# Kernel tuning notes

Measured on AMD Instinct MI355X. Metric: run time of the kernel, lower is better.

The kernel has to match this reference:

```python
import jax, jax.numpy as jnp
import numpy as np
from jax import lax

TEMPERATURE = 30.0
BN_EPS = 1e-5


def setup_inputs() -> dict:
    key = jax.random.key(0)
    ks = jax.random.split(key, 9)
    B, H, W, C_in = 32, 64, 64, 128
    n_filters, r_filters, n_kernels = 128, 4, 4
    x = jax.random.normal(ks[0], (B, H, W, C_in), dtype=jnp.float32)
    reduction_kernel = jax.random.normal(ks[1], (C_in, r_filters), dtype=jnp.float32) * 0.02
    attention_kernel = jax.random.normal(ks[2], (r_filters, n_kernels), dtype=jnp.float32) * 0.02
    conv_kernels = jax.random.normal(ks[3], (n_kernels, 3, 3, C_in, n_filters), dtype=jnp.float32) * 0.05
    bias = jax.random.normal(ks[4], (n_kernels, n_filters), dtype=jnp.float32) * 0.05
    bn_scale = jax.random.uniform(ks[5], (n_filters,), dtype=jnp.float32, minval=0.5, maxval=1.5)
    bn_bias = jax.random.normal(ks[6], (n_filters,), dtype=jnp.float32) * 0.1
    bn_mean = jax.random.normal(ks[7], (n_filters,), dtype=jnp.float32) * 0.1
    bn_var = jax.random.uniform(ks[8], (n_filters,), dtype=jnp.float32, minval=0.5, maxval=1.5)
    return {"x": x, "reduction_kernel": reduction_kernel, "attention_kernel": attention_kernel,
            "conv_kernels": conv_kernels, "bias": bias, "bn_scale": bn_scale, "bn_bias": bn_bias,
            "bn_mean": bn_mean, "bn_var": bn_var}


def reference(x, reduction_kernel, attention_kernel, conv_kernels, bias, bn_scale, bn_bias, bn_mean, bn_var):
    # x: [B,H,W,C_in] NHWC. Inference mode (training=False): BN uses running stats.
    B = x.shape[0]
    # Squeeze-style routing: global average pool -> reduce -> relu -> attention over experts.
    pool = jnp.mean(x, axis=(1, 2))                             # [B, C_in]
    pool_red = jax.nn.relu(pool @ reduction_kernel)             # [B, r]
    attention = jax.nn.softmax((pool_red @ attention_kernel) / TEMPERATURE, axis=-1)  # [B, K]
    # Soft mixture of conv expert kernels, per sample.
    w_mixed = jnp.einsum('bk,khwio->bhwio', attention, conv_kernels)  # [B,kH,kW,C_in,F]

    def per_sample_conv(xi, wi):
        # xi: [H,W,C_in], wi: [kH,kW,C_in,F]
        return lax.conv_general_dilated(xi[None], wi, window_strides=(1, 1), padding='SAME',
                                        dimension_numbers=('NHWC', 'HWIO', 'NHWC'))[0]

    y = jax.vmap(per_sample_conv)(x, w_mixed)                   # [B,H,W,F]
    b_mixed = attention @ bias                                  # [B, F]
    y = y + b_mixed[:, None, None, :]
    # BatchNorm (inference) + relu
    inv = bn_scale * lax.rsqrt(bn_var + BN_EPS)
    y = (y - bn_mean) * inv + bn_bias
    return jax.nn.relu(y)
```

## Files before the change

### kernel.cpp

```cpp
#include <hip/hip_runtime.h>

typedef short bf16x8 __attribute__((ext_vector_type(8)));
typedef float f32x4 __attribute__((ext_vector_type(4)));
typedef unsigned int u32x4 __attribute__((ext_vector_type(4)));
typedef unsigned short u16x4 __attribute__((ext_vector_type(4)));

__device__ __forceinline__ unsigned short f2bf(float f) {
  unsigned u = __builtin_bit_cast(unsigned, f);
  u = (u + 0x7FFFu + ((u >> 16) & 1u)) >> 16;
  return (unsigned short)u;
}

__global__ __launch_bounds__(256) void k_pool_cvt(const float* __restrict__ x,
                                                  unsigned short* __restrict__ xb,
                                                  float* __restrict__ pp) {
  const int slice = blockIdx.x;
  const int b = blockIdx.y;
  const int t = threadIdx.x;
  const int c4 = (t & 31) * 4;
  const int seg = t >> 5;
  const size_t base = ((size_t)b * 4096 + slice * 256 + seg * 32) * 128;
  const float* xp = x + base;
  unsigned short* xbp = xb + base;
  f32x4 s = {0.f, 0.f, 0.f, 0.f};
  for (int p = 0; p < 32; ++p) {
    f32x4 v = *(const f32x4*)(xp + p * 128 + c4);
    s += v;
    u16x4 h;
    h.x = f2bf(v.x); h.y = f2bf(v.y); h.z = f2bf(v.z); h.w = f2bf(v.w);
    *(u16x4*)(xbp + p * 128 + c4) = h;
  }
  __shared__ f32x4 red[256];
  red[t] = s;
  __syncthreads();
  if (t < 32) {
    f32x4 tot = red[t];
#pragma unroll
    for (int g = 1; g < 8; ++g) tot += red[g * 32 + t];
    *(f32x4*)(pp + (size_t)(b * 16 + slice) * 128 + t * 4) = tot;
  }
}

__global__ __launch_bounds__(128) void k_route(const float* __restrict__ pp,
    const float* __restrict__ redk, const float* __restrict__ attk,
    const float* __restrict__ bias, const float* __restrict__ bns,
    const float* __restrict__ bnb, const float* __restrict__ bnm,
    const float* __restrict__ bnv,
    float* __restrict__ att_ws, float* __restrict__ beta_ws,
    float* __restrict__ alpha_ws) {
  const int b = blockIdx.x, t = threadIdx.x;
  __shared__ float pool[128];
  __shared__ float att[4];
  {
    float s = 0.f;
    for (int i = 0; i < 16; ++i) s += pp[(size_t)(b * 16 + i) * 128 + t];
    pool[t] = s * (1.f / 4096.f);
  }
  __syncthreads();
  if (t == 0) {
    float pr[4];
    for (int r = 0; r < 4; ++r) {
      float s = 0.f;
      for (int c = 0; c < 128; ++c) s += pool[c] * redk[c * 4 + r];
      pr[r] = fmaxf(s, 0.f);
    }
    float lgt[4]; float mx = -1e30f;
    for (int k = 0; k < 4; ++k) {
      float s = 0.f;
      for (int r = 0; r < 4; ++r) s += pr[r] * attk[r * 4 + k];
      lgt[k] = s * (1.f / 30.f);
      mx = fmaxf(mx, lgt[k]);
    }
    float den = 0.f;
    for (int k = 0; k < 4; ++k) { lgt[k] = expf(lgt[k] - mx); den += lgt[k]; }
    for (int k = 0; k < 4; ++k) { att[k] = lgt[k] / den; att_ws[b * 4 + k] = att[k]; }
  }
  __syncthreads();
  {
    float bm = 0.f;
    for (int k = 0; k < 4; ++k) bm += att[k] * bias[k * 128 + t];
    const float inv = bns[t] * rsqrtf(bnv[t] + 1e-5f);
    beta_ws[b * 128 + t] = (bm - bnm[t]) * inv + bnb[t];
    alpha_ws[t] = inv;
  }
}

__global__ __launch_bounds__(256) void k_mixw(const float* __restrict__ ck,
                                              const float* __restrict__ att_ws,
                                              unsigned short* __restrict__ w_ws) {
  const int tap = blockIdx.x;
  const int b = blockIdx.y;
  const int t = threadIdx.x;
  const float a0 = att_ws[b * 4 + 0], a1 = att_ws[b * 4 + 1];
  const float a2 = att_ws[b * 4 + 2], a3 = att_ws[b * 4 + 3];
  const float* ckp = ck + (size_t)tap * 16384;
  __shared__ unsigned short lds_t[128 * 136];
#pragma unroll 4
  for (int it = 0; it < 16; ++it) {
    const int i4 = t + it * 256;
    const int idx = i4 * 4;
    const int c = idx >> 7, f = idx & 127;
    f32x4 v0 = *(const f32x4*)(ckp + idx);
    f32x4 v1 = *(const f32x4*)(ckp + idx + 147456);
    f32x4 v2 = *(const f32x4*)(ckp + idx + 2 * 147456);
    f32x4 v3 = *(const f32x4*)(ckp + idx + 3 * 147456);
#pragma unroll
    for (int e = 0; e < 4; ++e)
      lds_t[(f + e) * 136 + c] = f2bf(a0 * v0[e] + a1 * v1[e] + a2 * v2[e] + a3 * v3[e]);
  }
  __syncthreads();
#pragma unroll
  for (int it = 0; it < 8; ++it) {
    const int m = t + it * 256;
    const int f = m >> 4, oo = m & 15, h = oo >> 3, o = oo & 7;
    unsigned short* dst = w_ws + ((size_t)b * 18 + h * 9 + tap) * 8192
                        + (size_t)(f * 8 + (o ^ (f & 7))) * 8;
    *(bf16x8*)dst = *(const bf16x8*)(lds_t + f * 136 + oo * 8);
  }
}

__device__ __forceinline__ void stage_w16(char* dst, const unsigned short* src, int t) {
#pragma unroll
  for (int j = 0; j < 2; ++j) {
    const int i = t + j * 512;
    __builtin_amdgcn_global_load_lds(
        (const __attribute__((address_space(1))) void*)(src + (size_t)i * 8),
        (__attribute__((address_space(3))) void*)(dst + i * 16), 16, 0, 0);
  }
}

__device__ __forceinline__ void stage_x_half(char* xt, const unsigned short* xbp,
                                             int r0, int h, int t) {
  const int pix = t >> 3;
  const int oct = (t & 7) ^ ((t >> 3) & 7);
#pragma unroll
  for (int j = 0; j < 6; ++j) {
    const int rr = r0 - 1 + j;
    char* dst = xt + j * 8192 + t * 16;
    if ((unsigned)rr < 64u) {
      __builtin_amdgcn_global_load_lds(
          (const __attribute__((address_space(1))) void*)
              (xbp + ((size_t)(rr * 64 + pix)) * 128 + h * 64 + oct * 8),
          (__attribute__((address_space(3))) void*)dst, 16, 0, 0);
    } else {
      *(u32x4*)dst = (u32x4){0, 0, 0, 0};
    }
  }
}

__global__ __launch_bounds__(512, 4) void k_conv(const unsigned short* __restrict__ xb,
                                                 const unsigned short* __restrict__ w_ws,
                                                 const float* __restrict__ alpha_ws,
                                                 const float* __restrict__ beta_ws,
                                                 float* __restrict__ out) {
  extern __shared__ char lds[];
  char* xt = lds;
  char* wlds = lds + 49152;

  const int orig = blockIdx.x;
  const int wg = (orig & 7) * 64 + (orig >> 3);
  const int b = wg >> 4;
  const int tile = wg & 15;
  const int t = threadIdx.x;
  const int lane = t & 63, wid = t >> 6;
  const int wm = wid >> 1, wn = wid & 1;
  const int lr = lane & 15, lg = lane >> 4;
  const int r0 = tile * 4;

  const unsigned short* xbp = xb + (size_t)b * 4096 * 128;
  const unsigned short* wsrc = w_ws + (size_t)b * 18 * 8192;

  f32x4 acc[4][4] = {};
  const bf16x8 zero = {};

  stage_x_half(xt, xbp, r0, 0, t);
  stage_w16(wlds, wsrc, t);
  __syncthreads();

  for (int s = 0; s < 18; ++s) {
    const int tap = s % 9;
    char* cb = wlds + ((s & 1) << 14);
    if (s < 17) stage_w16(wlds + (((s & 1) ^ 1) << 14), wsrc + (size_t)(s + 1) * 8192, t);
    const int dh = tap / 3 - 1, dw = tap % 3 - 1;
    const int jrow = wm + dh + 1;
#pragma unroll
    for (int kc = 0; kc < 2; ++kc) {
      bf16x8 afr[4], bfr[4];
#pragma unroll
      for (int mf = 0; mf < 4; ++mf) {
        const int col = mf * 16 + lr + dw;
        const int a = ((jrow * 64 + col) * 128 + kc * 64 + lg * 16) ^ ((col & 7) << 4);
        afr[mf] = ((unsigned)col < 64u) ? *(const bf16x8*)(xt + a) : zero;
      }
#pragma unroll
      for (int nf = 0; nf < 4; ++nf) {
        const int f = wn * 64 + nf * 16 + lr;
        const int a = (f * 128 + kc * 64 + lg * 16) ^ ((f & 7) << 4);
        bfr[nf] = *(const bf16x8*)(cb + a);
      }
#pragma unroll
      for (int mf = 0; mf < 4; ++mf)
#pragma unroll
        for (int nf = 0; nf < 4; ++nf)
          acc[mf][nf] = __builtin_amdgcn_mfma_f32_16x16x32_bf16(afr[mf], bfr[nf],
                                                                acc[mf][nf], 0, 0, 0);
    }
    __syncthreads();
    if (s == 8) {
      stage_x_half(xt, xbp, r0, 1, t);
      __syncthreads();
    }
  }

  float af[4], bt[4];
#pragma unroll
  for (int nf = 0; nf < 4; ++nf) {
    const int f = wn * 64 + nf * 16 + lr;
    af[nf] = alpha_ws[f];
    bt[nf] = beta_ws[b * 128 + f];
  }
  float* op = out + (size_t)b * 4096 * 128;
  const int row = r0 + wm;
#pragma unroll
  for (int mf = 0; mf < 4; ++mf) {
#pragma unroll
    for (int r = 0; r < 4; ++r) {
      const int col = mf * 16 + lg * 4 + r;
#pragma unroll
      for (int nf = 0; nf < 4; ++nf) {
        const int f = wn * 64 + nf * 16 + lr;
        const float v = acc[mf][nf][r] * af[nf] + bt[nf];
        op[(size_t)(row * 64 + col) * 128 + f] = fmaxf(v, 0.f);
      }
    }
  }
}

extern "C" void kernel_launch(void* const* d_in, const int* in_sizes, int n_in,
                              void* d_out, int out_size, void* d_ws, size_t ws_size,
                              hipStream_t stream) {
  const float* x    = (const float*)d_in[0];
  const float* redk = (const float*)d_in[1];
  const float* attk = (const float*)d_in[2];
  const float* ck   = (const float*)d_in[3];
  const float* bias = (const float*)d_in[4];
  const float* bns  = (const float*)d_in[5];
  const float* bnbb = (const float*)d_in[6];
  const float* bnm  = (const float*)d_in[7];
  const float* bnv  = (const float*)d_in[8];
  float* out = (float*)d_out;

  char* ws = (char*)d_ws;
  unsigned short* xb   = (unsigned short*)ws;
  unsigned short* w_ws = (unsigned short*)(ws + 33554432);
  float* pp       = (float*)(ws + 42991616);
  float* att_ws   = (float*)(ws + 43253760);
  float* beta_ws  = (float*)(ws + 43254272);
  float* alpha_ws = (float*)(ws + 43270656);

  k_pool_cvt<<<dim3(16, 32), 256, 0, stream>>>(x, xb, pp);
  k_route<<<32, 128, 0, stream>>>(pp, redk, attk, bias, bns, bnbb, bnm, bnv,
                                  att_ws, beta_ws, alpha_ws);
  k_mixw<<<dim3(9, 32), 256, 0, stream>>>(ck, att_ws, w_ws);
  k_conv<<<512, 512, 81920, stream>>>(xb, w_ws, alpha_ws, beta_ws, out);
}
```

Before: 83.15 us.

## Load conv weights directly from global into registers with double-buffered prefetch

The conv kernel no longer stages mixed weights through LDS. Each wave reads its B fragments straight from global (L2) memory into registers, with a two-deep register prefetch, and the weight workspace is relaid into per-k-chunk 32-element rows to suit this. The tile shrinks to 2 output rows with 256 threads and 1024 blocks, which cuts LDS to 32KB and the per-tap barriers to those around the x-half restage. The cost is more global/L2 traffic for weights, since each block re-reads its sample's full weight set, and exposed global latency if the prefetch does not hide it.

```diff
diff --git a/kernel.cpp b/kernel.cpp
--- a/kernel.cpp
+++ b/kernel.cpp
@@ -109,38 +109,35 @@
       lds_t[(f + e) * 136 + c] = f2bf(a0 * v0[e] + a1 * v1[e] + a2 * v2[e] + a3 * v3[e]);
   }
   __syncthreads();
+  unsigned short* wb = w_ws + (size_t)b * 147456;
 #pragma unroll
   for (int it = 0; it < 8; ++it) {
     const int m = t + it * 256;
-    const int f = m >> 4, oo = m & 15, h = oo >> 3, o = oo & 7;
-    unsigned short* dst = w_ws + ((size_t)b * 18 + h * 9 + tap) * 8192
-                        + (size_t)(f * 8 + (o ^ (f & 7))) * 8;
-    *(bf16x8*)dst = *(const bf16x8*)(lds_t + f * 136 + oo * 8);
-  }
-}
-
-__device__ __forceinline__ void stage_w16(char* dst, const unsigned short* src, int t) {
-#pragma unroll
-  for (int j = 0; j < 2; ++j) {
-    const int i = t + j * 512;
-    __builtin_amdgcn_global_load_lds(
-        (const __attribute__((address_space(1))) void*)(src + (size_t)i * 8),
-        (__attribute__((address_space(3))) void*)(dst + i * 16), 16, 0, 0);
-  }
-}
-
-__device__ __forceinline__ void stage_x_half(char* xt, const unsigned short* xbp,
-                                             int r0, int h, int t) {
-  const int pix = t >> 3;
-  const int oct = (t & 7) ^ ((t >> 3) & 7);
-#pragma unroll
-  for (int j = 0; j < 6; ++j) {
-    const int rr = r0 - 1 + j;
-    char* dst = xt + j * 8192 + t * 16;
+    const int f = m >> 4, o = m & 15;
+    const int h = o >> 3;
+    const int cp = (o & 7) * 8;
+    const int kc = cp >> 5;
+    const int c2 = cp & 31;
+    unsigned short* dst = wb + ((size_t)(((h * 9 + tap) * 2 + kc) * 128 + f)) * 32 + c2;
+    *(bf16x8*)dst = *(const bf16x8*)(lds_t + f * 136 + o * 8);
+  }
+}
+
+__device__ __forceinline__ void stage_x(char* xt, const unsigned short* xbp,
+                                        int r0, int h, int t) {
+#pragma unroll
+  for (int j = 0; j < 8; ++j) {
+    const int i = t + j * 256;
+    const int jr = i >> 9;
+    const int pix = (i & 511) >> 3;
+    const int oct = i & 7;
+    const int soct = oct ^ (pix & 7);
+    const int rr = r0 - 1 + jr;
+    char* dst = xt + i * 16;
     if ((unsigned)rr < 64u) {
       __builtin_amdgcn_global_load_lds(
           (const __attribute__((address_space(1))) void*)
-              (xbp + ((size_t)(rr * 64 + pix)) * 128 + h * 64 + oct * 8),
+              (xbp + ((size_t)(rr * 64 + pix)) * 128 + h * 64 + soct * 8),
           (__attribute__((address_space(3))) void*)dst, 16, 0, 0);
     } else {
       *(u32x4*)dst = (u32x4){0, 0, 0, 0};
@@ -148,66 +145,73 @@
   }
 }
 
-__global__ __launch_bounds__(512, 4) void k_conv(const unsigned short* __restrict__ xb,
+#define LOADB(dst, u)                                                          \
+  {                                                                            \
+    const unsigned short* wp = wsrc + (size_t)(u) * 4096;                      \
+    _Pragma("unroll")                                                          \
+    for (int nf = 0; nf < 4; ++nf) {                                           \
+      const int f = wn * 64 + nf * 16 + lr;                                    \
+      dst[nf] = *(const bf16x8*)(wp + f * 32 + lg * 8);                        \
+    }                                                                          \
+  }
+
+#define COMPUTE(kc, bfr)                                                       \
+  {                                                                            \
+    bf16x8 afr[4];                                                             \
+    _Pragma("unroll")                                                          \
+    for (int mf = 0; mf < 4; ++mf) {                                           \
+      const int col = mf * 16 + lr + dw;                                       \
+      const int a = (((jrow * 64 + col) * 128 + (kc) * 64 + lg * 16))          \
+                    ^ ((col & 7) << 4);                                        \
+      afr[mf] = ((unsigned)col < 64u) ? *(const bf16x8*)(xt + a) : zero;       \
+    }                                                                          \
+    _Pragma("unroll")                                                          \
+    for (int mf = 0; mf < 4; ++mf)                                             \
+      _Pragma("unroll")                                                        \
+      for (int nf = 0; nf < 4; ++nf)                                           \
+        acc[mf][nf] = __builtin_amdgcn_mfma_f32_16x16x32_bf16(afr[mf],         \
+                          bfr[nf], acc[mf][nf], 0, 0, 0);                      \
+  }
+
+__global__ __launch_bounds__(256, 3) void k_conv(const unsigned short* __restrict__ xb,
                                                  const unsigned short* __restrict__ w_ws,
                                                  const float* __restrict__ alpha_ws,
                                                  const float* __restrict__ beta_ws,
                                                  float* __restrict__ out) {
-  extern __shared__ char lds[];
-  char* xt = lds;
-  char* wlds = lds + 49152;
+  __shared__ char xt[32768];
 
   const int orig = blockIdx.x;
-  const int wg = (orig & 7) * 64 + (orig >> 3);
-  const int b = wg >> 4;
-  const int tile = wg & 15;
+  const int wg = (orig & 7) * 128 + (orig >> 3);
+  const int b = wg >> 5;
+  const int tile = wg & 31;
   const int t = threadIdx.x;
   const int lane = t & 63, wid = t >> 6;
   const int wm = wid >> 1, wn = wid & 1;
   const int lr = lane & 15, lg = lane >> 4;
-  const int r0 = tile * 4;
+  const int r0 = tile * 2;
 
   const unsigned short* xbp = xb + (size_t)b * 4096 * 128;
-  const unsigned short* wsrc = w_ws + (size_t)b * 18 * 8192;
+  const unsigned short* wsrc = w_ws + (size_t)b * 147456;
 
   f32x4 acc[4][4] = {};
   const bf16x8 zero = {};
-
-  stage_x_half(xt, xbp, r0, 0, t);
-  stage_w16(wlds, wsrc, t);
-  __syncthreads();
-
-  for (int s = 0; s < 18; ++s) {
-    const int tap = s % 9;
-    char* cb = wlds + ((s & 1) << 14);
-    if (s < 17) stage_w16(wlds + (((s & 1) ^ 1) << 14), wsrc + (size_t)(s + 1) * 8192, t);
+  bf16x8 bA[4], bB[4];
+
+  stage_x(xt, xbp, r0, 0, t);
+  LOADB(bA, 0);
+  __syncthreads();
+
+  for (int u = 0; u < 36; u += 2) {
+    const int tap = (u >> 1) % 9;
     const int dh = tap / 3 - 1, dw = tap % 3 - 1;
     const int jrow = wm + dh + 1;
-#pragma unroll
-    for (int kc = 0; kc < 2; ++kc) {
-      bf16x8 afr[4], bfr[4];
-#pragma unroll
-      for (int mf = 0; mf < 4; ++mf) {
-        const int col = mf * 16 + lr + dw;
-        const int a = ((jrow * 64 + col) * 128 + kc * 64 + lg * 16) ^ ((col & 7) << 4);
-        afr[mf] = ((unsigned)col < 64u) ? *(const bf16x8*)(xt + a) : zero;
-      }
-#pragma unroll
-      for (int nf = 0; nf < 4; ++nf) {
-        const int f = wn * 64 + nf * 16 + lr;
-        const int a = (f * 128 + kc * 64 + lg * 16) ^ ((f & 7) << 4);
-        bfr[nf] = *(const bf16x8*)(cb + a);
-      }
-#pragma unroll
-      for (int mf = 0; mf < 4; ++mf)
-#pragma unroll
-        for (int nf = 0; nf < 4; ++nf)
-          acc[mf][nf] = __builtin_amdgcn_mfma_f32_16x16x32_bf16(afr[mf], bfr[nf],
-                                                                acc[mf][nf], 0, 0, 0);
-    }
-    __syncthreads();
-    if (s == 8) {
-      stage_x_half(xt, xbp, r0, 1, t);
+    LOADB(bB, u + 1);
+    COMPUTE(0, bA);
+    LOADB(bA, (u + 2 < 36) ? (u + 2) : 35);
+    COMPUTE(1, bB);
+    if (u == 16) {
+      __syncthreads();
+      stage_x(xt, xbp, r0, 1, t);
       __syncthreads();
     }
   }
@@ -262,5 +266,5 @@
   k_route<<<32, 128, 0, stream>>>(pp, redk, attk, bias, bns, bnbb, bnm, bnv,
                                   att_ws, beta_ws, alpha_ws);
   k_mixw<<<dim3(9, 32), 256, 0, stream>>>(ck, att_ws, w_ws);
-  k_conv<<<512, 512, 81920, stream>>>(xb, w_ws, alpha_ws, beta_ws, out);
-}
+  k_conv<<<1024, 256, 0, stream>>>(xb, w_ws, alpha_ws, beta_ws, out);
+}
```

Result: slower. 86.50 us (+4.0%).
